# Kernel optimization log

Hardware: AMD Instinct MI355X
Metric: run time of the kernel (lower is better)

## Reference

```python
import jax, jax.numpy as jnp
import numpy as np

NUM_NODES = 100000
HIDDEN = 128
HEADS = 4
NUM_EDGES = 1600000
NUM_PAIRS = 100000


def _leaky_relu(x, slope=0.2):
    return jnp.where(x >= 0, x, slope * x)


def _gat_layer(x, W, a_src, a_dst, src, dst):
    # x: [N, D]; W: [D, H*Dh]; a_src/a_dst: [H, Dh]
    N = x.shape[0]
    H, Dh = a_src.shape
    h = (x @ W).reshape(N, H, Dh)
    hs = h[src]                                   # [E, H, Dh] gather
    e = _leaky_relu((hs * a_src).sum(-1) + (h[dst] * a_dst).sum(-1))  # [E, H]
    # torch scatter_reduce amax over a zeros buffer => max clamped at 0
    m = jnp.maximum(jax.ops.segment_max(e, dst, num_segments=N), 0.0)  # [N, H]
    a = jnp.exp(e - m[dst])
    s = jax.ops.segment_sum(a, dst, num_segments=N)
    a = a / (s[dst] + 1e-10)
    out = jax.ops.segment_sum(hs * a[..., None], dst, num_segments=N)  # [N, H, Dh]
    return out.reshape(N, H * Dh)


def setup_inputs() -> dict:
    key = jax.random.key(0)
    ks = jax.random.split(key, 16)
    N, D, H = NUM_NODES, HIDDEN, HEADS
    Dh = D // H
    sW = float(np.sqrt(6.0 / (D + D)))
    sa = float(np.sqrt(6.0 / (H + Dh)))
    inp = {
        'embed': jax.random.uniform(ks[0], (N, D), jnp.float32, -sW, sW),
        'W1': jax.random.uniform(ks[1], (D, D), jnp.float32, -sW, sW),
        'a_src1': jax.random.uniform(ks[2], (H, Dh), jnp.float32, -sa, sa),
        'a_dst1': jax.random.uniform(ks[3], (H, Dh), jnp.float32, -sa, sa),
        'W2': jax.random.uniform(ks[4], (D, D), jnp.float32, -sW, sW),
        'a_src2': jax.random.uniform(ks[5], (H, Dh), jnp.float32, -sa, sa),
        'a_dst2': jax.random.uniform(ks[6], (H, Dh), jnp.float32, -sa, sa),
        'lp_w1': jax.random.uniform(ks[7], (2 * D, D), jnp.float32, -sW, sW),
        'lp_b1': jnp.zeros((D,), jnp.float32),
        'lp_w2': jax.random.uniform(ks[8], (D, 1), jnp.float32, -sW, sW),
        'lp_b2': jnp.zeros((1,), jnp.float32),
        'edge_index': jax.random.randint(ks[9], (2, NUM_EDGES), 0, N, jnp.int64 if jax.config.jax_enable_x64 else jnp.int32),
        'link_src': jax.random.randint(ks[10], (NUM_PAIRS,), 0, N),
        'link_dst': jax.random.randint(ks[11], (NUM_PAIRS,), 0, N),
    }
    return inp


def reference(embed, W1, a_src1, a_dst1, W2, a_src2, a_dst2,
              lp_w1, lp_b1, lp_w2, lp_b2, edge_index, link_src, link_dst):
    src, dst = edge_index[0], edge_index[1]
    x = embed
    x = jax.nn.elu(_gat_layer(x, W1, a_src1, a_dst1, src, dst)) + x
    x = jax.nn.elu(_gat_layer(x, W2, a_src2, a_dst2, src, dst)) + x
    z = x
    hcat = jnp.concatenate([z[link_src], z[link_dst]], axis=-1)  # [P, 2D]
    hid = jax.nn.relu(hcat @ lp_w1 + lp_b1)
    logits = (hid @ lp_w2 + lp_b2).squeeze(-1)  # [P]
    return logits
```

## Files before the change

kernel.cpp:

```cpp
#include <hip/hip_runtime.h>

typedef unsigned short u16;
typedef unsigned int u32;
typedef __attribute__((ext_vector_type(8))) short short8;
typedef __attribute__((ext_vector_type(4))) float float4v;

#define N_NODES 100000
#define N_EDGES 1600000
#define N_PAIRS 100000
#define NBUCK 391
#define BUCK_CAP 4608
#define BIN_GRID 391

__device__ __forceinline__ float bf2f(u32 lo16) {
    union { u32 u; float f; } v;
    v.u = lo16 << 16;
    return v.f;
}
__device__ __forceinline__ u16 f2bf(float f) {
    union { float f; u32 u; } v;
    v.f = f;
    u32 r = v.u + 0x7fffu + ((v.u >> 16) & 1u);
    return (u16)(r >> 16);
}

#define FMIX_LO(A, Q, W) asm("v_fma_mix_f32 %0, %1, %2, %0 op_sel:[0,0,0] op_sel_hi:[1,1,0]" : "+v"(A) : "v"(Q), "v"(W))
#define FMIX_HI(A, Q, W) asm("v_fma_mix_f32 %0, %1, %2, %0 op_sel:[1,0,0] op_sel_hi:[1,1,0]" : "+v"(A) : "v"(Q), "v"(W))

__global__ __launch_bounds__(256) void k_prepB4(const float* __restrict__ W1, const float* __restrict__ W2,
                                                const float* __restrict__ WA, const float* __restrict__ WB,
                                                u16* __restrict__ B1, u16* __restrict__ B2,
                                                u16* __restrict__ BA, u16* __restrict__ BB,
                                                int* __restrict__ bucket_cur) {
    if (blockIdx.x == 32) {
        for (int i = threadIdx.x; i < NBUCK; i += 256)
            bucket_cur[i] = i * BUCK_CAP;
        return;
    }
    int w = blockIdx.x >> 3;
    const float* W = (w == 0) ? W1 : (w == 1) ? W2 : (w == 2) ? WA : WB;
    u16* Bf = (w == 0) ? B1 : (w == 1) ? B2 : (w == 2) ? BA : BB;
    int t = (blockIdx.x & 7) * 256 + threadIdx.x;
    int kk = t >> 9, tn = (t >> 6) & 7, quad = (t >> 4) & 3, l15 = t & 15;
#pragma unroll
    for (int j = 0; j < 8; j++) {
        int k = kk * 32 + quad * 8 + j;
        int n = tn * 16 + l15;
        Bf[(size_t)t * 8 + j] = f2bf(W[k * 128 + n]);
    }
}

__global__ __launch_bounds__(256) void k_bin(const int* __restrict__ esrc, const int* __restrict__ edst,
                                             int* bucket_cur, u32* __restrict__ binned) {
    __shared__ int cnt[NBUCK];
    __shared__ int base[NBUCK];
    int t = threadIdx.x;
    for (int i = t; i < NBUCK; i += 256) cnt[i] = 0;
    __syncthreads();
    int s[16], d[16], r[16];
    int e0 = blockIdx.x * 4096;
#pragma unroll
    for (int k = 0; k < 16; k++) {
        int e = e0 + k * 256 + t;
        if (e < N_EDGES) {
            s[k] = esrc[e];
            d[k] = edst[e];
            r[k] = atomicAdd(&cnt[d[k] >> 8], 1);
        } else {
            d[k] = -1;
        }
    }
    __syncthreads();
    for (int i = t; i < NBUCK; i += 256)
        base[i] = cnt[i] ? atomicAdd(&bucket_cur[i], cnt[i]) : 0;
    __syncthreads();
#pragma unroll
    for (int k = 0; k < 16; k++) {
        if (d[k] >= 0) {
            int bk = d[k] >> 8;
            int pos = base[bk] + r[k];
            if (pos < (bk + 1) * BUCK_CAP)
                binned[pos] = ((u32)s[k] << 8) | ((u32)d[k] & 255u);
        }
    }
}

__global__ __launch_bounds__(256) void k_sort(const u32* __restrict__ binned,
                                              const int* __restrict__ bucket_cur,
                                              int* __restrict__ row_ptr,
                                              int* __restrict__ col_src) {
    __shared__ int cnt[256];
    __shared__ int sm[256];
    int b = blockIdx.x, t = threadIdx.x;

    int partial = 0;
    for (int i = t; i < b; i += 256) {
        int c = bucket_cur[i] - i * BUCK_CAP;
        partial += (c > BUCK_CAP) ? BUCK_CAP : c;
    }
    sm[t] = partial;
    __syncthreads();
    for (int o = 128; o >= 1; o >>= 1) {
        if (t < o) sm[t] += sm[t + o];
        __syncthreads();
    }
    int base = sm[0];
    int n_e = bucket_cur[b] - b * BUCK_CAP;
    if (n_e > BUCK_CAP) n_e = BUCK_CAP;
    __syncthreads();

    cnt[t] = 0;
    __syncthreads();
    const u32* ebase = binned + (size_t)b * BUCK_CAP;
    u32 ed[18];
#pragma unroll
    for (int j = 0; j < 18; j++) {
        int i = t + j * 256;
        ed[j] = (i < n_e) ? ebase[i] : 0xFFFFFFFFu;
        if (ed[j] != 0xFFFFFFFFu) atomicAdd(&cnt[ed[j] & 255u], 1);
    }
    __syncthreads();
    int v = cnt[t];
    sm[t] = v;
    __syncthreads();
    for (int o = 1; o < 256; o <<= 1) {
        int x = (t >= o) ? sm[t - o] : 0;
        __syncthreads();
        sm[t] += x;
        __syncthreads();
    }
    int excl = base + sm[t] - v;
    int node = b * 256 + t;
    if (node <= N_NODES) row_ptr[node] = excl;
    cnt[t] = excl;
    __syncthreads();
#pragma unroll
    for (int j = 0; j < 18; j++) {
        if (ed[j] != 0xFFFFFFFFu) {
            int p = atomicAdd(&cnt[ed[j] & 255u], 1);
            col_src[p] = (int)(ed[j] >> 8);
        }
    }
}

template<bool AF32, bool QUANT>
__global__ __launch_bounds__(256) void k_gemm(const void* __restrict__ Ap,
                                              const u16* __restrict__ Bf,
                                              u16* __restrict__ C,
                                              char* __restrict__ hq,
                                              float* __restrict__ alsc,
                                              const float* __restrict__ a_src,
                                              const float* __restrict__ a_dst,
                                              float* __restrict__ al_d, int M) {
    int wave = threadIdx.x >> 6, lane = threadIdx.x & 63;
    int quad = lane >> 4, l15 = lane & 15;
    int row0 = blockIdx.x * 64 + wave * 16;
    int m = row0 + l15;
    int mload = (m < M) ? m : (M - 1);

    short8 a[4];
    if (AF32) {
        const float* A = (const float*)Ap;
#pragma unroll
        for (int kk = 0; kk < 4; kk++) {
            const float* p = A + (size_t)mload * 128 + kk * 32 + quad * 8;
            float4 f0 = *(const float4*)p;
            float4 f1 = *(const float4*)(p + 4);
            short8 av;
            av[0] = (short)f2bf(f0.x); av[1] = (short)f2bf(f0.y);
            av[2] = (short)f2bf(f0.z); av[3] = (short)f2bf(f0.w);
            av[4] = (short)f2bf(f1.x); av[5] = (short)f2bf(f1.y);
            av[6] = (short)f2bf(f1.z); av[7] = (short)f2bf(f1.w);
            a[kk] = av;
        }
    } else {
        const u16* A = (const u16*)Ap;
#pragma unroll
        for (int kk = 0; kk < 4; kk++)
            a[kk] = *(const short8*)(A + (size_t)mload * 128 + kk * 32 + quad * 8);
    }

    float4v acc[8];
#pragma unroll
    for (int tn = 0; tn < 8; tn++) acc[tn] = (float4v){0.f, 0.f, 0.f, 0.f};

#pragma unroll
    for (int kk = 0; kk < 4; kk++) {
#pragma unroll
        for (int tn = 0; tn < 8; tn++) {
            short8 b = *(const short8*)(Bf + ((size_t)((kk * 8 + tn) * 64 + lane)) * 8);
            acc[tn] = __builtin_amdgcn_mfma_f32_16x16x32_bf16(a[kk], b, acc[tn], 0, 0, 0);
        }
    }

    float as0[4], as1[4], ad0[4], ad1[4];
    if (QUANT) {
#pragma unroll
        for (int hd = 0; hd < 4; hd++) {
            as0[hd] = a_src[hd * 32 + l15];
            as1[hd] = a_src[hd * 32 + 16 + l15];
            ad0[hd] = a_dst[hd * 32 + l15];
            ad1[hd] = a_dst[hd * 32 + 16 + l15];
        }
    }

#pragma unroll
    for (int rg = 0; rg < 4; rg++) {
        int gr = row0 + quad * 4 + rg;
        bool ok = (gr < M);
        if (!QUANT) {
            if (ok) {
#pragma unroll
                for (int tn = 0; tn < 8; tn++)
                    C[(size_t)gr * 128 + tn * 16 + l15] = f2bf(acc[tn][rg]);
            }
        } else {
            float amax = 0.f;
#pragma unroll
            for (int tn = 0; tn < 8; tn++) amax = fmaxf(amax, fabsf(acc[tn][rg]));
#pragma unroll
            for (int mm = 1; mm < 16; mm <<= 1) amax = fmaxf(amax, __shfl_xor(amax, mm, 64));
            float inv_s = (amax > 0.f) ? 127.f / amax : 0.f;
            if (ok) {
#pragma unroll
                for (int tn = 0; tn < 8; tn++) {
                    int q = (int)rintf(acc[tn][rg] * inv_s);
                    hq[(size_t)gr * 128 + tn * 16 + l15] = (char)(q + 128);
                }
            }
            float ps[4], pd[4];
#pragma unroll
            for (int hd = 0; hd < 4; hd++) {
                float c0 = acc[2 * hd][rg];
                float c1 = acc[2 * hd + 1][rg];
                ps[hd] = c0 * as0[hd] + c1 * as1[hd];
                pd[hd] = c0 * ad0[hd] + c1 * ad1[hd];
            }
#pragma unroll
            for (int mm = 1; mm < 16; mm <<= 1) {
#pragma unroll
                for (int hd = 0; hd < 4; hd++) {
                    ps[hd] += __shfl_xor(ps[hd], mm, 64);
                    pd[hd] += __shfl_xor(pd[hd], mm, 64);
                }
            }
            if (ok && l15 < 4) {
                float vs = (l15 == 0) ? ps[0] : (l15 == 1) ? ps[1] : (l15 == 2) ? ps[2] : ps[3];
                float vd = (l15 == 0) ? pd[0] : (l15 == 1) ? pd[1] : (l15 == 2) ? pd[2] : pd[3];
                alsc[(size_t)gr * 8 + l15 * 2]     = vs;
                alsc[(size_t)gr * 8 + l15 * 2 + 1] = amax * (1.f / 127.f);
                al_d[gr * 4 + l15] = vd;
            }
        }
    }
}

template<bool XF32>
__global__ __launch_bounds__(256) void k_agg(const int* __restrict__ row_ptr, const int* __restrict__ col_src,
                      const float* __restrict__ alsc, const float* __restrict__ al_d,
                      const char* __restrict__ hq,
                      const void* __restrict__ xin, u16* __restrict__ xout) {
    int node = blockIdx.x * 4 + (threadIdx.x >> 6);
    int lane = threadIdx.x & 63;
    int l15 = lane & 15;
    int grp = lane >> 4;
    int bh  = l15 >> 2;
    int ae  = lane >> 2;
    int ah  = lane & 3;
    int beg = row_ptr[node], end = row_ptr[node + 1];
    int deg = end - beg;
    int degm1 = (deg > 0) ? deg - 1 : 0;
    float adst = al_d[node * 4 + ah];
    u32 loff = (u32)(l15 * 8);

    float sw = 0.f, swl = 0.f;
    u32 h_one = 0x3C00u;
    float acc[8];
#pragma unroll
    for (int k = 0; k < 8; k++) acc[k] = 0.f;

    int nch = (deg + 15) >> 4;
    for (int cb = 0; cb < nch; cb++) {
        int c = cb * 16;
        int idx = c + l15;
        idx = (idx <= degm1) ? idx : degm1;
        int sv = col_src[beg + idx];

        int sA = __shfl(sv, ae, 64);
        float2 av = *(const float2*)(alsc + ((size_t)sA << 3) + (ah << 1));
        float ev = av.x + adst;
        ev = fmaxf(ev, 0.2f * ev);
        float w = __expf(ev);
        w = ((c + ae) < deg) ? w : 0.f;
        sw += w;
        float wsc = w * av.y;

#pragma unroll
        for (int i = 0; i < 4; i++) {
            int slot = 4 * i + grp;
            int s = __shfl(sv, slot, 64);
            float wl = __shfl(wsc, slot * 4 + bh, 64);
            u32 wlh;
            asm("v_cvt_f16_f32 %0, %1" : "=v"(wlh) : "v"(wl));
            FMIX_LO(swl, h_one, wlh);
            u32 off = ((u32)s << 7) + loff;
            uint2 hv = *(const uint2*)(hq + off);
            u32 p01 = __builtin_amdgcn_perm(0x64646464u, hv.x, 0x04010400u);
            u32 p23 = __builtin_amdgcn_perm(0x64646464u, hv.x, 0x04030402u);
            u32 p45 = __builtin_amdgcn_perm(0x64646464u, hv.y, 0x04010400u);
            u32 p67 = __builtin_amdgcn_perm(0x64646464u, hv.y, 0x04030402u);
            FMIX_LO(acc[0], p01, wlh); FMIX_HI(acc[1], p01, wlh);
            FMIX_LO(acc[2], p23, wlh); FMIX_HI(acc[3], p23, wlh);
            FMIX_LO(acc[4], p45, wlh); FMIX_HI(acc[5], p45, wlh);
            FMIX_LO(acc[6], p67, wlh); FMIX_HI(acc[7], p67, wlh);
        }
    }

#pragma unroll
    for (int k = 0; k < 8; k++) acc[k] = fmaf(swl, -1152.f, acc[k]);

#pragma unroll
    for (int mm = 4; mm < 64; mm <<= 1) sw += __shfl_xor(sw, mm, 64);
    float inv = 1.f / (__shfl(sw, bh, 64) + 1e-10f);

#pragma unroll
    for (int k = 0; k < 8; k++) {
        acc[k] += __shfl_xor(acc[k], 16, 64);
        acc[k] += __shfl_xor(acc[k], 32, 64);
    }

    if (grp == 0) {
        float r[8];
        if (XF32) {
            const float* x = (const float*)xin;
            float4 x0 = *(const float4*)&x[(size_t)node * 128 + l15 * 8];
            float4 x1 = *(const float4*)&x[(size_t)node * 128 + l15 * 8 + 4];
            r[0] = x0.x; r[1] = x0.y; r[2] = x0.z; r[3] = x0.w;
            r[4] = x1.x; r[5] = x1.y; r[6] = x1.z; r[7] = x1.w;
        } else {
            const u16* x = (const u16*)xin;
            short8 xv = *(const short8*)&x[(size_t)node * 128 + l15 * 8];
#pragma unroll
            for (int k = 0; k < 8; k++) r[k] = bf2f((u16)xv[k]);
        }
        u32 ow[4];
#pragma unroll
        for (int k = 0; k < 4; k++) {
            float a0 = acc[2 * k] * inv;
            float a1 = acc[2 * k + 1] * inv;
            a0 = (a0 > 0.f) ? a0 : (__expf(a0) - 1.f);
            a1 = (a1 > 0.f) ? a1 : (__expf(a1) - 1.f);
            ow[k] = (u32)f2bf(a0 + r[2 * k]) | ((u32)f2bf(a1 + r[2 * k + 1]) << 16);
        }
        *(uint4*)&xout[(size_t)node * 128 + l15 * 8] = make_uint4(ow[0], ow[1], ow[2], ow[3]);
    }
}

__global__ __launch_bounds__(256) void k_link(const int* __restrict__ psrc, const int* __restrict__ pdst,
                                              const u16* __restrict__ z,
                                              const u16* __restrict__ BfA, const u16* __restrict__ BfB,
                                              const float* __restrict__ b1, const float* __restrict__ w2,
                                              const float* __restrict__ b2, float* __restrict__ out) {
    int wave = threadIdx.x >> 6, lane = threadIdx.x & 63;
    int quad = lane >> 4, l15 = lane & 15;
    int row0 = blockIdx.x * 64 + wave * 16;
    int prow = row0 + l15;
    int pload = (prow < N_PAIRS) ? prow : (N_PAIRS - 1);
    int s = psrc[pload], d = pdst[pload];

    short8 a1[4], a2[4];
#pragma unroll
    for (int kk = 0; kk < 4; kk++) {
        a1[kk] = *(const short8*)(z + (size_t)s * 128 + kk * 32 + quad * 8);
        a2[kk] = *(const short8*)(z + (size_t)d * 128 + kk * 32 + quad * 8);
    }

    float4v acc[8];
#pragma unroll
    for (int tn = 0; tn < 8; tn++) acc[tn] = (float4v){0.f, 0.f, 0.f, 0.f};

#pragma unroll
    for (int kk = 0; kk < 4; kk++) {
#pragma unroll
        for (int tn = 0; tn < 8; tn++) {
            short8 ba = *(const short8*)(BfA + ((size_t)((kk * 8 + tn) * 64 + lane)) * 8);
            acc[tn] = __builtin_amdgcn_mfma_f32_16x16x32_bf16(a1[kk], ba, acc[tn], 0, 0, 0);
            short8 bb = *(const short8*)(BfB + ((size_t)((kk * 8 + tn) * 64 + lane)) * 8);
            acc[tn] = __builtin_amdgcn_mfma_f32_16x16x32_bf16(a2[kk], bb, acc[tn], 0, 0, 0);
        }
    }

    float b1v[8], w2v[8];
#pragma unroll
    for (int tn = 0; tn < 8; tn++) {
        b1v[tn] = b1[tn * 16 + l15];
        w2v[tn] = w2[tn * 16 + l15];
    }
    float bb2 = b2[0];

#pragma unroll
    for (int rg = 0; rg < 4; rg++) {
        float part = 0.f;
#pragma unroll
        for (int tn = 0; tn < 8; tn++) {
            float h = acc[tn][rg] + b1v[tn];
            h = (h > 0.f) ? h : 0.f;
            part += h * w2v[tn];
        }
#pragma unroll
        for (int mm = 1; mm < 16; mm <<= 1) part += __shfl_xor(part, mm, 64);
        int gr = row0 + quad * 4 + rg;
        if (l15 == 0 && gr < N_PAIRS) out[gr] = part + bb2;
    }
}

extern "C" void kernel_launch(void* const* d_in, const int* in_sizes, int n_in,
                              void* d_out, int out_size, void* d_ws, size_t ws_size,
                              hipStream_t stream) {
    const float* embed  = (const float*)d_in[0];
    const float* W1     = (const float*)d_in[1];
    const float* a_src1 = (const float*)d_in[2];
    const float* a_dst1 = (const float*)d_in[3];
    const float* W2     = (const float*)d_in[4];
    const float* a_src2 = (const float*)d_in[5];
    const float* a_dst2 = (const float*)d_in[6];
    const float* lp_w1  = (const float*)d_in[7];
    const float* lp_b1  = (const float*)d_in[8];
    const float* lp_w2  = (const float*)d_in[9];
    const float* lp_b2  = (const float*)d_in[10];
    const int*   edge   = (const int*)d_in[11];
    const int*   lsrc   = (const int*)d_in[12];
    const int*   ldst   = (const int*)d_in[13];
    float* out = (float*)d_out;

    char* ws = (char*)d_ws;
    size_t off = 0;
    auto alloc = [&](size_t bytes) -> char* {
        char* p = ws + off;
        off += (bytes + 255) & ~(size_t)255;
        return p;
    };
    int*  row_ptr    = (int*)alloc((N_NODES + 1) * 4);
    int*  bucket_cur = (int*)alloc(512 * 4);
    u32*  binned     = (u32*)alloc((size_t)NBUCK * BUCK_CAP * 4);
    int*  col_src    = (int*)alloc((size_t)N_EDGES * 4);
    char* hq         = (char*)alloc((size_t)N_NODES * 128);
    float* alsc      = (float*)alloc((size_t)N_NODES * 8 * 4);
    float* al_d      = (float*)alloc((size_t)N_NODES * 4 * 4);
    u16*  x1         = (u16*)alloc((size_t)N_NODES * 128 * 2);
    u16*  z          = (u16*)alloc((size_t)N_NODES * 128 * 2);
    u16*  Bf1        = (u16*)alloc(128 * 128 * 2);
    u16*  Bf2        = (u16*)alloc(128 * 128 * 2);
    u16*  BfA        = (u16*)alloc(128 * 128 * 2);
    u16*  BfB        = (u16*)alloc(128 * 128 * 2);

    const int* esrc = edge;
    const int* edst = edge + N_EDGES;
    const int GB = (N_NODES + 63) / 64;
    const int GP = (N_PAIRS + 63) / 64;

    k_prepB4<<<33, 256, 0, stream>>>(W1, W2, lp_w1, lp_w1 + 128 * 128, Bf1, Bf2, BfA, BfB, bucket_cur);

    k_bin <<<BIN_GRID, 256, 0, stream>>>(esrc, edst, bucket_cur, binned);
    k_sort<<<NBUCK, 256, 0, stream>>>(binned, bucket_cur, row_ptr, col_src);

    k_gemm<true, true><<<GB, 256, 0, stream>>>(embed, Bf1, nullptr,
                                               hq, alsc, a_src1, a_dst1, al_d, N_NODES);
    k_agg<true><<<N_NODES / 4, 256, 0, stream>>>(row_ptr, col_src, alsc, al_d, hq, embed, x1);
    k_gemm<false, true><<<GB, 256, 0, stream>>>(x1, Bf2, nullptr,
                                                hq, alsc, a_src2, a_dst2, al_d, N_NODES);
    k_agg<false><<<N_NODES / 4, 256, 0, stream>>>(row_ptr, col_src, alsc, al_d, hq, x1, z);
    k_link<<<GP, 256, 0, stream>>>(lsrc, ldst, z, BfA, BfB, lp_b1, lp_w2, lp_b2, out);
}
```

Baseline: 326.0 us.

## Merge prep with binning and CSR sort with first GEMM into combined launches

Weight conversion and edge binning now run as block ranges of one kernel, and the CSR sort shares a launch with the first-layer GEMM, since these pairs are independent. Bucket counters become zero-based via a memset instead of being set in the prep kernel. This removes two kernel launches and the gaps between them, and lets independent work overlap on the GPU. In exchange, the merged kernels need the register and shared-memory budget of the larger body, which may lower occupancy for the other one.

```diff
diff --git a/kernel.cpp b/kernel.cpp
--- a/kernel.cpp
+++ b/kernel.cpp
@@ -27,20 +27,16 @@
 #define FMIX_LO(A, Q, W) asm("v_fma_mix_f32 %0, %1, %2, %0 op_sel:[0,0,0] op_sel_hi:[1,1,0]" : "+v"(A) : "v"(Q), "v"(W))
 #define FMIX_HI(A, Q, W) asm("v_fma_mix_f32 %0, %1, %2, %0 op_sel:[1,0,0] op_sel_hi:[1,1,0]" : "+v"(A) : "v"(Q), "v"(W))
 
-__global__ __launch_bounds__(256) void k_prepB4(const float* __restrict__ W1, const float* __restrict__ W2,
-                                                const float* __restrict__ WA, const float* __restrict__ WB,
-                                                u16* __restrict__ B1, u16* __restrict__ B2,
-                                                u16* __restrict__ BA, u16* __restrict__ BB,
-                                                int* __restrict__ bucket_cur) {
-    if (blockIdx.x == 32) {
-        for (int i = threadIdx.x; i < NBUCK; i += 256)
-            bucket_cur[i] = i * BUCK_CAP;
-        return;
-    }
-    int w = blockIdx.x >> 3;
+
+__device__ __forceinline__ void prep_body(int blk, int tid,
+                                          const float* __restrict__ W1, const float* __restrict__ W2,
+                                          const float* __restrict__ WA, const float* __restrict__ WB,
+                                          u16* __restrict__ B1, u16* __restrict__ B2,
+                                          u16* __restrict__ BA, u16* __restrict__ BB) {
+    int w = blk >> 3;
     const float* W = (w == 0) ? W1 : (w == 1) ? W2 : (w == 2) ? WA : WB;
     u16* Bf = (w == 0) ? B1 : (w == 1) ? B2 : (w == 2) ? BA : BB;
-    int t = (blockIdx.x & 7) * 256 + threadIdx.x;
+    int t = (blk & 7) * 256 + tid;
     int kk = t >> 9, tn = (t >> 6) & 7, quad = (t >> 4) & 3, l15 = t & 15;
 #pragma unroll
     for (int j = 0; j < 8; j++) {
@@ -50,15 +46,15 @@
     }
 }
 
-__global__ __launch_bounds__(256) void k_bin(const int* __restrict__ esrc, const int* __restrict__ edst,
-                                             int* bucket_cur, u32* __restrict__ binned) {
+__device__ __forceinline__ void bin_body(int blk, int t,
+                                         const int* __restrict__ esrc, const int* __restrict__ edst,
+                                         int* bucket_cur, u32* __restrict__ binned) {
     __shared__ int cnt[NBUCK];
     __shared__ int base[NBUCK];
-    int t = threadIdx.x;
     for (int i = t; i < NBUCK; i += 256) cnt[i] = 0;
     __syncthreads();
     int s[16], d[16], r[16];
-    int e0 = blockIdx.x * 4096;
+    int e0 = blk * 4096;
 #pragma unroll
     for (int k = 0; k < 16; k++) {
         int e = e0 + k * 256 + t;
@@ -79,23 +75,23 @@
         if (d[k] >= 0) {
             int bk = d[k] >> 8;
             int pos = base[bk] + r[k];
-            if (pos < (bk + 1) * BUCK_CAP)
-                binned[pos] = ((u32)s[k] << 8) | ((u32)d[k] & 255u);
-        }
-    }
-}
-
-__global__ __launch_bounds__(256) void k_sort(const u32* __restrict__ binned,
-                                              const int* __restrict__ bucket_cur,
-                                              int* __restrict__ row_ptr,
-                                              int* __restrict__ col_src) {
+            if (pos < BUCK_CAP)
+                binned[(size_t)bk * BUCK_CAP + pos] = ((u32)s[k] << 8) | ((u32)d[k] & 255u);
+        }
+    }
+}
+
+__device__ __forceinline__ void sort_body(int b, int t,
+                                          const u32* __restrict__ binned,
+                                          const int* __restrict__ bucket_cur,
+                                          int* __restrict__ row_ptr,
+                                          int* __restrict__ col_src) {
     __shared__ int cnt[256];
     __shared__ int sm[256];
-    int b = blockIdx.x, t = threadIdx.x;
 
     int partial = 0;
     for (int i = t; i < b; i += 256) {
-        int c = bucket_cur[i] - i * BUCK_CAP;
+        int c = bucket_cur[i];
         partial += (c > BUCK_CAP) ? BUCK_CAP : c;
     }
     sm[t] = partial;
@@ -105,7 +101,7 @@
         __syncthreads();
     }
     int base = sm[0];
-    int n_e = bucket_cur[b] - b * BUCK_CAP;
+    int n_e = bucket_cur[b];
     if (n_e > BUCK_CAP) n_e = BUCK_CAP;
     __syncthreads();
 
@@ -144,17 +140,18 @@
 }
 
 template<bool AF32, bool QUANT>
-__global__ __launch_bounds__(256) void k_gemm(const void* __restrict__ Ap,
-                                              const u16* __restrict__ Bf,
-                                              u16* __restrict__ C,
-                                              char* __restrict__ hq,
-                                              float* __restrict__ alsc,
-                                              const float* __restrict__ a_src,
-                                              const float* __restrict__ a_dst,
-                                              float* __restrict__ al_d, int M) {
-    int wave = threadIdx.x >> 6, lane = threadIdx.x & 63;
+__device__ __forceinline__ void gemm_body(int bid, int tid,
+                                          const void* __restrict__ Ap,
+                                          const u16* __restrict__ Bf,
+                                          u16* __restrict__ C,
+                                          char* __restrict__ hq,
+                                          float* __restrict__ alsc,
+                                          const float* __restrict__ a_src,
+                                          const float* __restrict__ a_dst,
+                                          float* __restrict__ al_d, int M) {
+    int wave = tid >> 6, lane = tid & 63;
     int quad = lane >> 4, l15 = lane & 15;
-    int row0 = blockIdx.x * 64 + wave * 16;
+    int row0 = bid * 64 + wave * 16;
     int m = row0 + l15;
     int mload = (m < M) ? m : (M - 1);
 
@@ -253,6 +250,39 @@
             }
         }
     }
+}
+
+__global__ __launch_bounds__(256) void k_prep_bin(const float* __restrict__ W1, const float* __restrict__ W2,
+                                                  const float* __restrict__ WA, const float* __restrict__ WB,
+                                                  u16* __restrict__ B1, u16* __restrict__ B2,
+                                                  u16* __restrict__ BA, u16* __restrict__ BB,
+                                                  const int* __restrict__ esrc, const int* __restrict__ edst,
+                                                  int* bucket_cur, u32* __restrict__ binned) {
+    if (blockIdx.x < 32)
+        prep_body(blockIdx.x, threadIdx.x, W1, W2, WA, WB, B1, B2, BA, BB);
+    else
+        bin_body(blockIdx.x - 32, threadIdx.x, esrc, edst, bucket_cur, binned);
+}
+
+__global__ __launch_bounds__(256) void k_sort_gemm1(const u32* __restrict__ binned,
+                                                    const int* __restrict__ bucket_cur,
+                                                    int* __restrict__ row_ptr, int* __restrict__ col_src,
+                                                    const float* __restrict__ embed, const u16* __restrict__ Bf1,
+                                                    char* __restrict__ hq, float* __restrict__ alsc,
+                                                    const float* __restrict__ a_src1, const float* __restrict__ a_dst1,
+                                                    float* __restrict__ al_d) {
+    if (blockIdx.x < NBUCK)
+        sort_body(blockIdx.x, threadIdx.x, binned, bucket_cur, row_ptr, col_src);
+    else
+        gemm_body<true, true>(blockIdx.x - NBUCK, threadIdx.x, embed, Bf1, nullptr,
+                              hq, alsc, a_src1, a_dst1, al_d, N_NODES);
+}
+
+__global__ __launch_bounds__(256) void k_gemm2(const u16* __restrict__ Ap, const u16* __restrict__ Bf,
+                                               char* __restrict__ hq, float* __restrict__ alsc,
+                                               const float* __restrict__ a_src, const float* __restrict__ a_dst,
+                                               float* __restrict__ al_d) {
+    gemm_body<false, true>(blockIdx.x, threadIdx.x, Ap, Bf, nullptr, hq, alsc, a_src, a_dst, al_d, N_NODES);
 }
 
 template<bool XF32>
@@ -459,16 +489,17 @@
     const int GB = (N_NODES + 63) / 64;
     const int GP = (N_PAIRS + 63) / 64;
 
-    k_prepB4<<<33, 256, 0, stream>>>(W1, W2, lp_w1, lp_w1 + 128 * 128, Bf1, Bf2, BfA, BfB, bucket_cur);
-
-    k_bin <<<BIN_GRID, 256, 0, stream>>>(esrc, edst, bucket_cur, binned);
-    k_sort<<<NBUCK, 256, 0, stream>>>(binned, bucket_cur, row_ptr, col_src);
-
-    k_gemm<true, true><<<GB, 256, 0, stream>>>(embed, Bf1, nullptr,
-                                               hq, alsc, a_src1, a_dst1, al_d, N_NODES);
+    hipMemsetAsync(bucket_cur, 0, NBUCK * sizeof(int), stream);
+
+    k_prep_bin<<<32 + BIN_GRID, 256, 0, stream>>>(W1, W2, lp_w1, lp_w1 + 128 * 128,
+                                                  Bf1, Bf2, BfA, BfB,
+                                                  esrc, edst, bucket_cur, binned);
+
+    k_sort_gemm1<<<NBUCK + GB, 256, 0, stream>>>(binned, bucket_cur, row_ptr, col_src,
+                                                 embed, Bf1, hq, alsc, a_src1, a_dst1, al_d);
+
     k_agg<true><<<N_NODES / 4, 256, 0, stream>>>(row_ptr, col_src, alsc, al_d, hq, embed, x1);
-    k_gemm<false, true><<<GB, 256, 0, stream>>>(x1, Bf2, nullptr,
-                                                hq, alsc, a_src2, a_dst2, al_d, N_NODES);
+    k_gemm2<<<GB, 256, 0, stream>>>(x1, Bf2, hq, alsc, a_src2, a_dst2, al_d);
     k_agg<false><<<N_NODES / 4, 256, 0, stream>>>(row_ptr, col_src, alsc, al_d, hq, x1, z);
     k_link<<<GP, 256, 0, stream>>>(lsrc, ldst, z, BfA, BfB, lp_b1, lp_w2, lp_b2, out);
 }
```

New measurement: 325.2 us. No clear change (-0.2%).
